# Optimization experiments

Hardware: AMD Instinct MI355X
Metric: run time of the kernel (lower is better)

The kernel has to match this reference:

```python
import jax, jax.numpy as jnp
import numpy as np

B, T, D, L, H = 8, 1024, 768, 8, 12
BLOCK_SIZE = 4
HD = D // H


def setup_inputs() -> dict:
    key = jax.random.key(0)
    ks = jax.random.split(key, 10)
    sd = 0.02
    return {
        "x_init": jax.random.normal(ks[0], (B, T, D), jnp.float32),
        "attn_proj_w": jax.random.normal(ks[1], (L, D), jnp.float32) * sd,
        "mlp_proj_w": jax.random.normal(ks[2], (L, D), jnp.float32) * sd,
        "Wqkv": jax.random.normal(ks[3], (L, D, 3 * D), jnp.float32) * sd,
        "Wo": jax.random.normal(ks[4], (L, D, D), jnp.float32) * sd,
        "Wm1": jax.random.normal(ks[5], (L, D, 4 * D), jnp.float32) * sd,
        "Wm2": jax.random.normal(ks[6], (L, 4 * D, D), jnp.float32) * sd,
        "attn_scale": 1.0 + jax.random.normal(ks[7], (L, D), jnp.float32) * sd,
        "mlp_scale": 1.0 + jax.random.normal(ks[8], (L, D), jnp.float32) * sd,
        "ln_s": jnp.ones((L,), jnp.float32),
    }


def _rms_norm(x):
    # F.rms_norm with eps=None -> eps = finfo(dtype).eps
    eps = jnp.finfo(x.dtype).eps
    return x * jax.lax.rsqrt(jnp.mean(x * x, axis=-1, keepdims=True) + eps)


def _aggregate(V, q):
    # V: [n, B, T, D]; scalar-query depth attention (keys RMS-normed, values raw)
    K = _rms_norm(V)
    logits = jnp.einsum('d,nbtd->nbt', q, K)
    w = jax.nn.softmax(logits, axis=0)
    return jnp.einsum('nbt,nbtd->btd', w, V)


def _mha(x, wqkv, wo):
    # causal multi-head self-attention
    b, t, d = x.shape
    qkv = x @ wqkv                                   # [b, t, 3D]
    q, k, v = jnp.split(qkv, 3, axis=-1)
    q = q.reshape(b, t, H, HD)
    k = k.reshape(b, t, H, HD)
    v = v.reshape(b, t, H, HD)
    scores = jnp.einsum('bqhd,bkhd->bhqk', q, k) / np.sqrt(HD).astype(np.float32)
    mask = jnp.tril(jnp.ones((t, t), bool))
    scores = jnp.where(mask[None, None], scores, jnp.asarray(-1e30, scores.dtype))
    attn = jax.nn.softmax(scores, axis=-1)
    out = jnp.einsum('bhqk,bkhd->bqhd', attn, v).reshape(b, t, d)
    return out @ wo


def reference(x_init, attn_proj_w, mlp_proj_w, Wqkv, Wo, Wm1, Wm2,
              attn_scale, mlp_scale, ln_s):
    boundary_every = max(1, BLOCK_SIZE // 2)
    hist = [x_init]          # committed block representations
    partial = x_init         # intra-block partial accumulator
    for l in range(L):
        s = ln_s[l]
        V = jnp.stack(hist + [partial], axis=0)          # [n_hist+1, B, T, D]
        h = _aggregate(V, attn_proj_w[l])
        if l % boundary_every == 0:
            hist.append(partial)
            partial = jnp.zeros_like(partial)
        attn_out = _mha(_rms_norm(h) * s, Wqkv[l], Wo[l])
        partial = partial + attn_scale[l][None, None, :] * attn_out
        V2 = jnp.stack(hist + [partial], axis=0)
        h = _aggregate(V2, mlp_proj_w[l])
        mlp_out = jax.nn.gelu((_rms_norm(h) * s) @ Wm1[l]) @ Wm2[l]
        partial = partial + mlp_scale[l][None, None, :] * mlp_out
    return partial
```

## Files before the change

### kernel.cpp

```cpp
#include <hip/hip_runtime.h>
#include <hip/hip_bf16.h>
#include <math.h>
#include <stdint.h>

#define D_MODEL 768
#define T_SEQ   1024
#define B_BATCH 8
#define NHEAD   12
#define HDIM    64
#define NLAYER  8

typedef unsigned short u16;
typedef __attribute__((ext_vector_type(8))) short bf16x8;
typedef __attribute__((ext_vector_type(4))) float f32x4;
typedef __attribute__((ext_vector_type(4))) uint32_t u32x4;

static constexpr size_t BTD  = (size_t)B_BATCH * T_SEQ * D_MODEL;
static constexpr int    ROWS = B_BATCH * T_SEQ;
static constexpr float  EPSF = 1.1920928955078125e-07f;


__device__ __forceinline__ u16 f2bf(float x) {
    __hip_bfloat16 h = __float2bfloat16(x);
    return __builtin_bit_cast(u16, h);
}
__device__ __forceinline__ float bf2f(u16 u) {
    __hip_bfloat16 h = __builtin_bit_cast(__hip_bfloat16, u);
    return __bfloat162float(h);
}
__device__ __forceinline__ void split_bf(float x, u16& hi, u16& lo) {
    hi = f2bf(x);
    lo = f2bf(x - bf2f(hi));
}
__device__ __forceinline__ uint32_t cvt_pk_bf16(float a, float b) {
    uint32_t r;
    asm("v_cvt_pk_bf16_f32 %0, %1, %2" : "=v"(r) : "v"(a), "v"(b));
    return r;
}
__device__ __forceinline__ f32x4 mfma16(bf16x8 a, bf16x8 b, f32x4 c) {
    return __builtin_amdgcn_mfma_f32_16x16x32_bf16(a, b, c, 0, 0, 0);
}

__device__ __forceinline__ void gl_lds16(const void* g, void* l) {
    auto gp = reinterpret_cast<const __attribute__((address_space(1))) char*>(
        reinterpret_cast<uintptr_t>(g));
    auto lp = reinterpret_cast<__attribute__((address_space(3))) char*>(
        static_cast<uint32_t>(reinterpret_cast<uintptr_t>(l)));
    __builtin_amdgcn_global_load_lds(gp, lp, 16, 0, 0);
}

__device__ __forceinline__ float block_reduce_sum(float v, float* sbuf) {
    #pragma unroll
    for (int off = 32; off > 0; off >>= 1) v += __shfl_down(v, off);
    __syncthreads();
    if ((threadIdx.x & 63) == 0) sbuf[threadIdx.x >> 6] = v;
    __syncthreads();
    return sbuf[0] + sbuf[1] + sbuf[2] + sbuf[3];
}

__device__ __forceinline__ float gelu_fast(float x) {
    float z = 0.7978845608028654f * (x + 0.044715f * x * x * x);
    float e = __expf(2.f * z);
    return x - x / (e + 1.f);
}

template<int N>
__global__ __launch_bounds__(256)
void agg_norm_kernel(const float* __restrict__ v0, const float* __restrict__ v1,
                     const float* __restrict__ v2, const float* __restrict__ v3,
                     const float* __restrict__ v4, const float* __restrict__ v5,
                     const float* __restrict__ q,  const float* __restrict__ lns,
                     u16* __restrict__ xh) {
    __shared__ float sbuf[4];
    const float* V[6] = {v0, v1, v2, v3, v4, v5};
    const size_t row = blockIdx.x;
    const int tid = threadIdx.x;

    float qv[3];
    #pragma unroll
    for (int j = 0; j < 3; ++j) qv[j] = q[tid + j * 256];

    float vv[N][3];
    float logits[N];
    #pragma unroll
    for (int i = 0; i < N; ++i) {
        const float* vr = V[i] + row * D_MODEL;
        float ssq = 0.f, qd = 0.f;
        #pragma unroll
        for (int j = 0; j < 3; ++j) {
            float x = vr[tid + j * 256];
            vv[i][j] = x;
            ssq = fmaf(x, x, ssq);
            qd  = fmaf(qv[j], x, qd);
        }
        float S  = block_reduce_sum(ssq, sbuf);
        float Qd = block_reduce_sum(qd,  sbuf);
        logits[i] = Qd * rsqrtf(S * (1.f / 768.f) + EPSF);
    }
    float mx = logits[0];
    #pragma unroll
    for (int i = 1; i < N; ++i) mx = fmaxf(mx, logits[i]);
    float w[N];
    float wsum = 0.f;
    #pragma unroll
    for (int i = 0; i < N; ++i) { w[i] = __expf(logits[i] - mx); wsum += w[i]; }
    float inv = 1.f / wsum;

    float outv[3] = {0.f, 0.f, 0.f};
    #pragma unroll
    for (int i = 0; i < N; ++i) {
        float wi = w[i] * inv;
        #pragma unroll
        for (int j = 0; j < 3; ++j) outv[j] = fmaf(wi, vv[i][j], outv[j]);
    }
    float ssq = 0.f;
    #pragma unroll
    for (int j = 0; j < 3; ++j) ssq = fmaf(outv[j], outv[j], ssq);
    float S2 = block_reduce_sum(ssq, sbuf);
    float scale = lns[0] * rsqrtf(S2 * (1.f / 768.f) + EPSF);
    #pragma unroll
    for (int j = 0; j < 3; ++j)
        xh[row * D_MODEL + tid + j * 256] = f2bf(outv[j] * scale);
}

__global__ __launch_bounds__(256)
void transpose_all(const float* __restrict__ Wqkv, const float* __restrict__ Wo,
                   const float* __restrict__ Wm1,  const float* __restrict__ Wm2,
                   u16* __restrict__ T0, u16* __restrict__ T1,
                   u16* __restrict__ T2, u16* __restrict__ T3) {
    const int id = blockIdx.x;
    const float* W; u16* Th; int K, N, t;
    if (id < 1728)      { W = Wqkv; Th = T0; K = 768;  N = 2304; t = id; }
    else if (id < 2304) { W = Wo;   Th = T1; K = 768;  N = 768;  t = id - 1728; }
    else if (id < 4608) { W = Wm1;  Th = T2; K = 768;  N = 3072; t = id - 2304; }
    else                { W = Wm2;  Th = T3; K = 3072; N = 768;  t = id - 4608; }
    const int nk = K >> 5;
    const int bk = (t % nk) * 32, bn = (t / nk) * 32;

    __shared__ float tt[32][33];
    const int r = threadIdx.x >> 3, c4 = (threadIdx.x & 7) * 4;
    float4 v = *(const float4*)&W[(size_t)(bk + r) * N + bn + c4];
    tt[r][c4 + 0] = v.x; tt[r][c4 + 1] = v.y; tt[r][c4 + 2] = v.z; tt[r][c4 + 3] = v.w;
    __syncthreads();
    u16 h[4];
    #pragma unroll
    for (int j = 0; j < 4; ++j) h[j] = f2bf(tt[c4 + j][r]);
    size_t o = (size_t)(bn + r) * K + bk + c4;
    *(uint2*)&Th[o] = make_uint2((uint32_t)h[0] | ((uint32_t)h[1] << 16),
                                 (uint32_t)h[2] | ((uint32_t)h[3] << 16));
}

__global__ __launch_bounds__(256)
void vt_transpose(const u16* __restrict__ vh, u16* __restrict__ vth) {
    __shared__ u16 th[32][36];
    const int bh = blockIdx.z;
    const int t0 = blockIdx.x * 32, d0 = blockIdx.y * 32;
    const int r = threadIdx.x >> 3, c = (threadIdx.x & 7) * 4;
    const size_t ib = ((size_t)(bh << 10) + t0 + r) * 64 + d0 + c;
    *(uint2*)&th[r][c] = *(const uint2*)&vh[ib];
    __syncthreads();
    const size_t ob = ((size_t)(bh << 6) + d0 + r) * 1024 + t0 + c;
    u16 a0 = th[c + 0][r], a1 = th[c + 1][r], a2 = th[c + 2][r], a3 = th[c + 3][r];
    *(uint2*)&vth[ob] = make_uint2((uint32_t)a0 | ((uint32_t)a1 << 16),
                                   (uint32_t)a2 | ((uint32_t)a3 << 16));
}

template<int EPI, int BN>
__global__ __launch_bounds__(256)
void gemm_bf1(const u16* __restrict__ Ah, const u16* __restrict__ Bh,
              float* __restrict__ Cf, u16* __restrict__ Ch,
              const float* __restrict__ scale, int M, int N, int K,
              u16* __restrict__ Qh, u16* __restrict__ Ql,
              u16* __restrict__ Kh, u16* __restrict__ Vh) {
    constexpr int NJ = BN / 32;
    constexpr int BUF_U16 = 4096 + BN * 32;
    __shared__ u16 smem[2 * BUF_U16];

    const int nwg = gridDim.x * gridDim.y;
    const int lin = blockIdx.y * gridDim.x + blockIdx.x;
    const int wg  = (lin & 7) * (nwg >> 3) + (lin >> 3);
    const int bm  = (wg / gridDim.x) << 7;
    const int bn  = (wg % gridDim.x) * BN;

    const int tid = threadIdx.x;
    const int w = tid >> 6, l = tid & 63;
    const int wr = w >> 1, wc = w & 1;

    const int grow = tid >> 2;
    const int gcol = (((tid & 3) ^ ((tid >> 3) & 3)) << 3);
    const size_t aoff0 = (size_t)(bm + grow) * K + gcol;
    const size_t boff0 = (size_t)(bn + grow) * K + gcol;
    const size_t s64 = (size_t)64 * K;
    char* sb0 = (char*)smem;
    char* sb1 = (char*)smem + 2 * BUF_U16;
    const uint32_t wq = (uint32_t)w << 10;

    auto stage = [&](char* sbuf, int k0) {
        gl_lds16(Ah + aoff0 + k0,       sbuf + 0    + wq);
        gl_lds16(Ah + aoff0 + s64 + k0, sbuf + 4096 + wq);
        gl_lds16(Bh + boff0 + k0,       sbuf + 8192 + wq);
        if constexpr (BN == 128)
            gl_lds16(Bh + boff0 + s64 + k0, sbuf + 12288 + wq);
    };

    f32x4 acc[4][NJ] = {};

    const int key8 = (((l & 15) >> 1) & 3) << 3;
    const int kswz = ((l >> 4) << 3) ^ key8;
    const int arow = wr * 64 + (l & 15);
    const int brow = wc * (BN / 2) + (l & 15);
    const int nk = K >> 5;

    stage(sb0, 0);
    for (int kt = 0; kt < nk; ++kt) {
        char* cur = (kt & 1) ? sb1 : sb0;
        char* nxt = (kt & 1) ? sb0 : sb1;
        if (kt + 1 < nk) {
            stage(nxt, (kt + 1) << 5);
            if constexpr (BN == 128)
                asm volatile("s_waitcnt vmcnt(4)\n\ts_barrier" ::: "memory");
            else
                asm volatile("s_waitcnt vmcnt(3)\n\ts_barrier" ::: "memory");
        } else {
            asm volatile("s_waitcnt vmcnt(0)\n\ts_barrier" ::: "memory");
        }
        __builtin_amdgcn_sched_barrier(0);

        const u16* bu = (const u16*)cur;
        bf16x8 ah[4], bh4[NJ];
        #pragma unroll
        for (int i = 0; i < 4; ++i)
            ah[i] = *(const bf16x8*)&bu[(arow + i * 16) * 32 + kswz];
        #pragma unroll
        for (int j = 0; j < NJ; ++j)
            bh4[j] = *(const bf16x8*)&bu[4096 + (brow + j * 16) * 32 + kswz];
        asm volatile("s_waitcnt lgkmcnt(0)" ::: "memory");
        __builtin_amdgcn_sched_barrier(0);
        asm volatile("s_barrier" ::: "memory");

        #pragma unroll
        for (int i = 0; i < 4; ++i) {
            #pragma unroll
            for (int j = 0; j < NJ; ++j)
                acc[i][j] = mfma16(ah[i], bh4[j], acc[i][j]);
        }
    }

    const int crow0 = bm + wr * 64 + ((l >> 4) << 2);
    const int ccol0 = bn + wc * (BN / 2) + (l & 15);
    #pragma unroll
    for (int i = 0; i < 4; ++i) {
        #pragma unroll
        for (int j = 0; j < NJ; ++j) {
            const int col = ccol0 + j * 16;
            #pragma unroll
            for (int r = 0; r < 4; ++r) {
                const int row = crow0 + i * 16 + r;
                const size_t o = (size_t)row * N + col;
                float v = acc[i][j][r];
                if (EPI == 1) {
                    Ch[o] = f2bf(gelu_fast(v));
                } else if (EPI == 2) {
                    Cf[o] += scale[col] * v;
                } else if (EPI == 4) {
                    Cf[o] = scale[col] * v;
                } else if (EPI == 3) {
                    const int which = (col >= 1536) ? 2 : ((col >= 768) ? 1 : 0);
                    const int hcol = col - which * 768;
                    const size_t dst = ((size_t)((row >> 10) * NHEAD + (hcol >> 6)) * 1024
                                        + (row & 1023)) * 64 + (hcol & 63);
                    if (which == 0) {
                        v *= 0.125f;
                        u16 hi, lo;
                        split_bf(v, hi, lo);
                        Qh[dst] = hi; Ql[dst] = lo;
                    } else if (which == 1) {
                        Kh[dst] = f2bf(v);
                    } else {
                        Vh[dst] = f2bf(v);
                    }
                }
            }
        }
    }
}

__global__ __launch_bounds__(256, 3)
void flash16(const u16* __restrict__ qh, const u16* __restrict__ ql,
             const u16* __restrict__ kh, const u16* __restrict__ vth,
             u16* __restrict__ ch) {
    const int id = blockIdx.x;
    const int r8 = id & 7, s = id >> 3;
    const int bh = r8 + 8 * (s >> 3);
    const int p  = s & 7;
    const int hh = bh % NHEAD, bb = bh / NHEAD;
    const int tid = threadIdx.x, w = tid >> 6, l = tid & 63;
    const int lq = l & 15, lg = l >> 4;
    const size_t hb = (size_t)bh << 16;

    const int wqA = p * 64 + w * 16;
    const int wqB = (15 - p) * 64 + w * 16;
    const int qA = wqA + lq, qB = wqB + lq;

    bf16x8 qA0, qA1, qA2, qA3, qB0, qB1, qB2, qB3;
    {
        const size_t qa = hb + ((size_t)qA << 6) + lg * 8;
        qA0 = *(const bf16x8*)(qh + qa);       qA1 = *(const bf16x8*)(ql + qa);
        qA2 = *(const bf16x8*)(qh + qa + 32);  qA3 = *(const bf16x8*)(ql + qa + 32);
        const size_t qb = hb + ((size_t)qB << 6) + lg * 8;
        qB0 = *(const bf16x8*)(qh + qb);       qB1 = *(const bf16x8*)(ql + qb);
        qB2 = *(const bf16x8*)(qh + qb + 32);  qB3 = *(const bf16x8*)(ql + qb + 32);
    }

    f32x4 oA[4] = {}, oB[4] = {};
    float mA = -30000.f, lsA = 0.f, mB = -30000.f, lsB = 0.f;
    const int ntiles = 32 - 2 * p;
    const int src0 = 32 * (lg & 1) + lq, src1 = src0 + 16;
    const bool hiHalf = lg >= 2;

    bf16x8 KA[4], KB[4], VA[4], VB[4];
    auto loadK = [&](bf16x8 (&K)[4], int k0) {
        const size_t kb0 = hb + (size_t)(k0 + lq) * 64 + lg * 8;
        const size_t kb1 = kb0 + 16 * 64;
        K[0] = *(const bf16x8*)(kh + kb0);
        K[1] = *(const bf16x8*)(kh + kb0 + 32);
        K[2] = *(const bf16x8*)(kh + kb1);
        K[3] = *(const bf16x8*)(kh + kb1 + 32);
    };
    auto loadV = [&](bf16x8 (&V)[4], int k0) {
        #pragma unroll
        for (int dt = 0; dt < 4; ++dt) {
            const size_t vb = hb + (size_t)(dt * 16 + lq) * 1024 + k0 + lg * 8;
            V[dt] = *(const bf16x8*)(vth + vb);
        }
    };

    auto path = [&](bf16x8 (&Kc)[4], bf16x8 (&vf)[4], int k0, int wqX, int qX,
                    bf16x8 q0, bf16x8 q1, bf16x8 q2, bf16x8 q3,
                    float& mX, float& lsX, f32x4 (&oX)[4]) {
        f32x4 s0 = {}, s1 = {};
        s0 = mfma16(Kc[0], q0, s0); s0 = mfma16(Kc[0], q1, s0);
        s0 = mfma16(Kc[1], q2, s0); s0 = mfma16(Kc[1], q3, s0);
        s1 = mfma16(Kc[2], q0, s1); s1 = mfma16(Kc[2], q1, s1);
        s1 = mfma16(Kc[3], q2, s1); s1 = mfma16(Kc[3], q3, s1);
        if (k0 + 31 > wqX) {
            #pragma unroll
            for (int r = 0; r < 4; ++r) {
                if (k0 + 4 * lg + r > qX)      s0[r] = -30000.f;
                if (k0 + 16 + 4 * lg + r > qX) s1[r] = -30000.f;
            }
        }
        float tmloc = fmaxf(fmaxf(fmaxf(s0[0], s0[1]), fmaxf(s0[2], s0[3])),
                            fmaxf(fmaxf(s1[0], s1[1]), fmaxf(s1[2], s1[3])));
        if (__any(tmloc > mX + 8.f)) {
            float tm = fmaxf(tmloc, __shfl_xor(tmloc, 16));
            tm = fmaxf(tm, __shfl_xor(tm, 32));
            const float mnew = fmaxf(mX, tm);
            const float fac = __expf(mX - mnew);
            mX = mnew;
            lsX *= fac;
            #pragma unroll
            for (int dt = 0; dt < 4; ++dt) {
                oX[dt][0] *= fac; oX[dt][1] *= fac;
                oX[dt][2] *= fac; oX[dt][3] *= fac;
            }
        }
        float ps = 0.f;
        #pragma unroll
        for (int r = 0; r < 4; ++r) {
            s0[r] = __expf(s0[r] - mX); ps += s0[r];
            s1[r] = __expf(s1[r] - mX); ps += s1[r];
        }
        lsX += ps;
        const uint32_t wA0 = cvt_pk_bf16(s0[0], s0[1]);
        const uint32_t wA1 = cvt_pk_bf16(s0[2], s0[3]);
        const uint32_t wB0 = cvt_pk_bf16(s1[0], s1[1]);
        const uint32_t wB1 = cvt_pk_bf16(s1[2], s1[3]);
        const uint32_t a0 = (uint32_t)__shfl((int)wA0, src0);
        const uint32_t b0 = (uint32_t)__shfl((int)wB0, src0);
        const uint32_t a1 = (uint32_t)__shfl((int)wA1, src0);
        const uint32_t b1 = (uint32_t)__shfl((int)wB1, src0);
        const uint32_t a2 = (uint32_t)__shfl((int)wA0, src1);
        const uint32_t b2 = (uint32_t)__shfl((int)wB0, src1);
        const uint32_t a3 = (uint32_t)__shfl((int)wA1, src1);
        const uint32_t b3 = (uint32_t)__shfl((int)wB1, src1);
        u32x4 pw = { hiHalf ? b0 : a0, hiHalf ? b1 : a1,
                     hiHalf ? b2 : a2, hiHalf ? b3 : a3 };
        const bf16x8 pb = __builtin_bit_cast(bf16x8, pw);
        #pragma unroll
        for (int dt = 0; dt < 4; ++dt)
            oX[dt] = mfma16(vf[dt], pb, oX[dt]);
    };

    auto step = [&](bf16x8 (&Kc)[4], bf16x8 (&Vc)[4],
                    bf16x8 (&Kn)[4], bf16x8 (&Vn)[4], int kt) {
        const int k0 = kt * 32;
        const int ktn = (kt + 1 < ntiles) ? kt + 1 : kt;
        loadK(Kn, ktn * 32);
        loadV(Vn, ktn * 32);
        if (k0 <= wqB + 15)
            path(Kc, Vc, k0, wqB, qB, qB0, qB1, qB2, qB3, mB, lsB, oB);
        if (k0 <= wqA + 15)
            path(Kc, Vc, k0, wqA, qA, qA0, qA1, qA2, qA3, mA, lsA, oA);
    };

    loadK(KA, 0);
    loadV(VA, 0);
    for (int kt = 0; kt < ntiles; kt += 2) {
        step(KA, VA, KB, VB, kt);
        step(KB, VB, KA, VA, kt + 1);
    }

    lsA += __shfl_xor(lsA, 16); lsA += __shfl_xor(lsA, 32);
    lsB += __shfl_xor(lsB, 16); lsB += __shfl_xor(lsB, 32);
    const float invA = 1.f / lsA, invB = 1.f / lsB;
    const size_t cbA = ((size_t)(bb * 1024 + qA)) * 768 + hh * 64;
    const size_t cbB = ((size_t)(bb * 1024 + qB)) * 768 + hh * 64;
    #pragma unroll
    for (int dt = 0; dt < 4; ++dt) {
        u16 h4[4];
        #pragma unroll
        for (int r = 0; r < 4; ++r) h4[r] = f2bf(oA[dt][r] * invA);
        size_t co = cbA + dt * 16 + 4 * lg;
        *(uint2*)&ch[co] = make_uint2((uint32_t)h4[0] | ((uint32_t)h4[1] << 16),
                                      (uint32_t)h4[2] | ((uint32_t)h4[3] << 16));
        #pragma unroll
        for (int r = 0; r < 4; ++r) h4[r] = f2bf(oB[dt][r] * invB);
        co = cbB + dt * 16 + 4 * lg;
        *(uint2*)&ch[co] = make_uint2((uint32_t)h4[0] | ((uint32_t)h4[1] << 16),
                                      (uint32_t)h4[2] | ((uint32_t)h4[3] << 16));
    }
}


extern "C" void kernel_launch(void* const* d_in, const int* in_sizes, int n_in,
                              void* d_out, int out_size, void* d_ws, size_t ws_size,
                              hipStream_t stream) {
    const float* x0     = (const float*)d_in[0];
    const float* aproj  = (const float*)d_in[1];
    const float* mproj  = (const float*)d_in[2];
    const float* Wqkv   = (const float*)d_in[3];
    const float* Wo     = (const float*)d_in[4];
    const float* Wm1    = (const float*)d_in[5];
    const float* Wm2    = (const float*)d_in[6];
    const float* ascale = (const float*)d_in[7];
    const float* mscale = (const float*)d_in[8];
    const float* lns    = (const float*)d_in[9];
    float* out = (float*)d_out;
    char*  base = (char*)d_ws;

    float* p1  = (float*)base;
    float* p2  = p1 + BTD;
    float* p3  = p2 + BTD;
    u16*   xnh = (u16*)(base + 12 * BTD);
    u16*   wt0 = (u16*)(base + 14 * BTD);
    u16*   wt1 = wt0 + (size_t)2304 * 768;
    u16*   wt2 = wt1 + (size_t)768 * 768;
    u16*   wt3 = wt2 + (size_t)3072 * 768;
    char*  QB  = (char*)(wt3 + (size_t)768 * 3072);
    u16* qh   = (u16*)QB;
    u16* ql   = qh  + BTD;
    u16* kh   = ql  + BTD;
    u16* vh   = kh  + BTD;
    u16* vth  = vh  + BTD;
    u16* ctxh = vh;
    u16* midh = qh;

    float* pb[3] = {p1, p2, p3};
    const float* hist[6];
    int nh = 1;
    hist[0] = x0;
    const float* partial_c = x0;
    float* partial_w = nullptr;
    int pidx = 0;

    auto launch_agg = [&](int n, const float* Vl6[6], const float* qvec,
                          const float* lnsl) {
        switch (n) {
        case 2: agg_norm_kernel<2><<<dim3(ROWS), 256, 0, stream>>>(Vl6[0], Vl6[1], Vl6[2], Vl6[3], Vl6[4], Vl6[5], qvec, lnsl, xnh); break;
        case 3: agg_norm_kernel<3><<<dim3(ROWS), 256, 0, stream>>>(Vl6[0], Vl6[1], Vl6[2], Vl6[3], Vl6[4], Vl6[5], qvec, lnsl, xnh); break;
        case 4: agg_norm_kernel<4><<<dim3(ROWS), 256, 0, stream>>>(Vl6[0], Vl6[1], Vl6[2], Vl6[3], Vl6[4], Vl6[5], qvec, lnsl, xnh); break;
        case 5: agg_norm_kernel<5><<<dim3(ROWS), 256, 0, stream>>>(Vl6[0], Vl6[1], Vl6[2], Vl6[3], Vl6[4], Vl6[5], qvec, lnsl, xnh); break;
        default: agg_norm_kernel<6><<<dim3(ROWS), 256, 0, stream>>>(Vl6[0], Vl6[1], Vl6[2], Vl6[3], Vl6[4], Vl6[5], qvec, lnsl, xnh); break;
        }
    };

    for (int l = 0; l < NLAYER; ++l) {
        transpose_all<<<dim3(6912), 256, 0, stream>>>(
            Wqkv + (size_t)l * D_MODEL * 3 * D_MODEL,
            Wo   + (size_t)l * D_MODEL * D_MODEL,
            Wm1  + (size_t)l * D_MODEL * 4 * D_MODEL,
            Wm2  + (size_t)l * 4 * D_MODEL * D_MODEL,
            wt0, wt1, wt2, wt3);

        const float* Vl6[6] = {nullptr, nullptr, nullptr, nullptr, nullptr, nullptr};
        for (int i = 0; i < nh; ++i) Vl6[i] = hist[i];
        Vl6[nh] = partial_c;
        launch_agg(nh + 1, Vl6, aproj + (size_t)l * D_MODEL, lns + l);

        const bool boundary = ((l & 1) == 0);
        if (boundary) {
            hist[nh++] = partial_c;
            float* np = (pidx < 3) ? pb[pidx] : out;
            ++pidx;
            partial_w = np;
            partial_c = np;
        }

        gemm_bf1<3, 128><<<dim3(3 * D_MODEL / 128, ROWS / 128), 256, 0, stream>>>(
            xnh, wt0, nullptr, nullptr, nullptr,
            ROWS, 3 * D_MODEL, D_MODEL, qh, ql, kh, vh);

        vt_transpose<<<dim3(T_SEQ / 32, HDIM / 32, B_BATCH * NHEAD), 256, 0, stream>>>(
            vh, vth);

        flash16<<<dim3(768), 256, 0, stream>>>(qh, ql, kh, vth, ctxh);

        if (boundary)
            gemm_bf1<4, 64><<<dim3(D_MODEL / 64, ROWS / 128), 256, 0, stream>>>(
                ctxh, wt1, partial_w, nullptr,
                ascale + (size_t)l * D_MODEL, ROWS, D_MODEL, D_MODEL,
                nullptr, nullptr, nullptr, nullptr);
        else
            gemm_bf1<2, 64><<<dim3(D_MODEL / 64, ROWS / 128), 256, 0, stream>>>(
                ctxh, wt1, partial_w, nullptr,
                ascale + (size_t)l * D_MODEL, ROWS, D_MODEL, D_MODEL,
                nullptr, nullptr, nullptr, nullptr);

        const float* V26[6] = {nullptr, nullptr, nullptr, nullptr, nullptr, nullptr};
        for (int i = 0; i < nh; ++i) V26[i] = hist[i];
        V26[nh] = partial_c;
        launch_agg(nh + 1, V26, mproj + (size_t)l * D_MODEL, lns + l);

        gemm_bf1<1, 128><<<dim3(4 * D_MODEL / 128, ROWS / 128), 256, 0, stream>>>(
            xnh, wt2, nullptr, midh,
            nullptr, ROWS, 4 * D_MODEL, D_MODEL,
            nullptr, nullptr, nullptr, nullptr);
        gemm_bf1<2, 64><<<dim3(D_MODEL / 64, ROWS / 128), 256, 0, stream>>>(
            midh, wt3, partial_w, nullptr,
            mscale + (size_t)l * D_MODEL, ROWS, D_MODEL, 4 * D_MODEL,
            nullptr, nullptr, nullptr, nullptr);
    }
}
```

Measured before the change: 2.862 ms.

## Deduplicate repeated aggregation inputs and split-K the second MLP GEMM

Because x_init is always present twice in the history, the aggregation kernel now reads it once and doubles its softmax weight. This removes one full-activation read per aggregation launch, and layer 0 takes a trivial single-input path. The down-projection GEMM (K=3072) is split into two K halves that accumulate into the residual with float atomics, doubling the block count. The atomics add read-modify-write traffic and make the summation order nondeterministic.

```diff
diff --git a/kernel.cpp b/kernel.cpp
--- a/kernel.cpp
+++ b/kernel.cpp
@@ -68,50 +68,58 @@
 __global__ __launch_bounds__(256)
 void agg_norm_kernel(const float* __restrict__ v0, const float* __restrict__ v1,
                      const float* __restrict__ v2, const float* __restrict__ v3,
-                     const float* __restrict__ v4, const float* __restrict__ v5,
+                     const float* __restrict__ v4,
                      const float* __restrict__ q,  const float* __restrict__ lns,
                      u16* __restrict__ xh) {
     __shared__ float sbuf[4];
-    const float* V[6] = {v0, v1, v2, v3, v4, v5};
+    const float* V[5] = {v0, v1, v2, v3, v4};
     const size_t row = blockIdx.x;
     const int tid = threadIdx.x;
 
-    float qv[3];
-    #pragma unroll
-    for (int j = 0; j < 3; ++j) qv[j] = q[tid + j * 256];
-
-    float vv[N][3];
-    float logits[N];
-    #pragma unroll
-    for (int i = 0; i < N; ++i) {
-        const float* vr = V[i] + row * D_MODEL;
-        float ssq = 0.f, qd = 0.f;
-        #pragma unroll
-        for (int j = 0; j < 3; ++j) {
-            float x = vr[tid + j * 256];
-            vv[i][j] = x;
-            ssq = fmaf(x, x, ssq);
-            qd  = fmaf(qv[j], x, qd);
-        }
-        float S  = block_reduce_sum(ssq, sbuf);
-        float Qd = block_reduce_sum(qd,  sbuf);
-        logits[i] = Qd * rsqrtf(S * (1.f / 768.f) + EPSF);
-    }
-    float mx = logits[0];
-    #pragma unroll
-    for (int i = 1; i < N; ++i) mx = fmaxf(mx, logits[i]);
-    float w[N];
-    float wsum = 0.f;
-    #pragma unroll
-    for (int i = 0; i < N; ++i) { w[i] = __expf(logits[i] - mx); wsum += w[i]; }
-    float inv = 1.f / wsum;
-
-    float outv[3] = {0.f, 0.f, 0.f};
-    #pragma unroll
-    for (int i = 0; i < N; ++i) {
-        float wi = w[i] * inv;
-        #pragma unroll
-        for (int j = 0; j < 3; ++j) outv[j] = fmaf(wi, vv[i][j], outv[j]);
+    float outv[3];
+    if constexpr (N == 1) {
+        #pragma unroll
+        for (int j = 0; j < 3; ++j) outv[j] = v0[row * D_MODEL + tid + j * 256];
+    } else {
+        float qv[3];
+        #pragma unroll
+        for (int j = 0; j < 3; ++j) qv[j] = q[tid + j * 256];
+
+        float vv[N][3];
+        float logits[N];
+        #pragma unroll
+        for (int i = 0; i < N; ++i) {
+            const float* vr = V[i] + row * D_MODEL;
+            float ssq = 0.f, qd = 0.f;
+            #pragma unroll
+            for (int j = 0; j < 3; ++j) {
+                float x = vr[tid + j * 256];
+                vv[i][j] = x;
+                ssq = fmaf(x, x, ssq);
+                qd  = fmaf(qv[j], x, qd);
+            }
+            float S  = block_reduce_sum(ssq, sbuf);
+            float Qd = block_reduce_sum(qd,  sbuf);
+            logits[i] = Qd * rsqrtf(S * (1.f / 768.f) + EPSF);
+        }
+        float mx = logits[0];
+        #pragma unroll
+        for (int i = 1; i < N; ++i) mx = fmaxf(mx, logits[i]);
+        float w[N];
+        #pragma unroll
+        for (int i = 0; i < N; ++i) w[i] = __expf(logits[i] - mx);
+        w[0] *= 2.f;
+        float wsum = 0.f;
+        #pragma unroll
+        for (int i = 0; i < N; ++i) wsum += w[i];
+        float inv = 1.f / wsum;
+        outv[0] = outv[1] = outv[2] = 0.f;
+        #pragma unroll
+        for (int i = 0; i < N; ++i) {
+            float wi = w[i] * inv;
+            #pragma unroll
+            for (int j = 0; j < 3; ++j) outv[j] = fmaf(wi, vv[i][j], outv[j]);
+        }
     }
     float ssq = 0.f;
     #pragma unroll
@@ -165,7 +173,7 @@
                                    (uint32_t)a2 | ((uint32_t)a3 << 16));
 }
 
-template<int EPI, int BN>
+template<int EPI, int BN, int KS>
 __global__ __launch_bounds__(256)
 void gemm_bf1(const u16* __restrict__ Ah, const u16* __restrict__ Bh,
               float* __restrict__ Cf, u16* __restrict__ Ch,
@@ -176,11 +184,13 @@
     constexpr int BUF_U16 = 4096 + BN * 32;
     __shared__ u16 smem[2 * BUF_U16];
 
-    const int nwg = gridDim.x * gridDim.y;
-    const int lin = blockIdx.y * gridDim.x + blockIdx.x;
+    const int gx = gridDim.x, gy = gridDim.y;
+    const int nwg = gx * gy * KS;
+    const int lin = (blockIdx.z * gy + blockIdx.y) * gx + blockIdx.x;
     const int wg  = (lin & 7) * (nwg >> 3) + (lin >> 3);
-    const int bm  = (wg / gridDim.x) << 7;
-    const int bn  = (wg % gridDim.x) * BN;
+    const int bn  = (wg % gx) * BN;
+    const int bm  = ((wg / gx) % gy) << 7;
+    const int kz  = wg / (gx * gy);
 
     const int tid = threadIdx.x;
     const int w = tid >> 6, l = tid & 63;
@@ -209,14 +219,15 @@
     const int kswz = ((l >> 4) << 3) ^ key8;
     const int arow = wr * 64 + (l & 15);
     const int brow = wc * (BN / 2) + (l & 15);
-    const int nk = K >> 5;
-
-    stage(sb0, 0);
-    for (int kt = 0; kt < nk; ++kt) {
+    const int nk2 = (K >> 5) / KS;
+    const int kt0 = kz * nk2;
+
+    stage(sb0, kt0 << 5);
+    for (int kt = 0; kt < nk2; ++kt) {
         char* cur = (kt & 1) ? sb1 : sb0;
         char* nxt = (kt & 1) ? sb0 : sb1;
-        if (kt + 1 < nk) {
-            stage(nxt, (kt + 1) << 5);
+        if (kt + 1 < nk2) {
+            stage(nxt, (kt0 + kt + 1) << 5);
             if constexpr (BN == 128)
                 asm volatile("s_waitcnt vmcnt(4)\n\ts_barrier" ::: "memory");
             else
@@ -264,6 +275,8 @@
                     Cf[o] += scale[col] * v;
                 } else if (EPI == 4) {
                     Cf[o] = scale[col] * v;
+                } else if (EPI == 5) {
+                    unsafeAtomicAdd(&Cf[o], scale[col] * v);
                 } else if (EPI == 3) {
                     const int which = (col >= 1536) ? 2 : ((col >= 768) ? 1 : 0);
                     const int hcol = col - which * 768;
@@ -467,21 +480,23 @@
     u16* midh = qh;
 
     float* pb[3] = {p1, p2, p3};
-    const float* hist[6];
-    int nh = 1;
-    hist[0] = x0;
-    const float* partial_c = x0;
+    const float* L[5] = {x0, nullptr, nullptr, nullptr, nullptr};
+    int nL = 1;
     float* partial_w = nullptr;
     int pidx = 0;
 
-    auto launch_agg = [&](int n, const float* Vl6[6], const float* qvec,
-                          const float* lnsl) {
-        switch (n) {
-        case 2: agg_norm_kernel<2><<<dim3(ROWS), 256, 0, stream>>>(Vl6[0], Vl6[1], Vl6[2], Vl6[3], Vl6[4], Vl6[5], qvec, lnsl, xnh); break;
-        case 3: agg_norm_kernel<3><<<dim3(ROWS), 256, 0, stream>>>(Vl6[0], Vl6[1], Vl6[2], Vl6[3], Vl6[4], Vl6[5], qvec, lnsl, xnh); break;
-        case 4: agg_norm_kernel<4><<<dim3(ROWS), 256, 0, stream>>>(Vl6[0], Vl6[1], Vl6[2], Vl6[3], Vl6[4], Vl6[5], qvec, lnsl, xnh); break;
-        case 5: agg_norm_kernel<5><<<dim3(ROWS), 256, 0, stream>>>(Vl6[0], Vl6[1], Vl6[2], Vl6[3], Vl6[4], Vl6[5], qvec, lnsl, xnh); break;
-        default: agg_norm_kernel<6><<<dim3(ROWS), 256, 0, stream>>>(Vl6[0], Vl6[1], Vl6[2], Vl6[3], Vl6[4], Vl6[5], qvec, lnsl, xnh); break;
+    auto launch_agg = [&](const float* qvec, const float* lnsl) {
+        const float* a = L[0];
+        const float* b = (nL > 1) ? L[1] : nullptr;
+        const float* c = (nL > 2) ? L[2] : nullptr;
+        const float* d = (nL > 3) ? L[3] : nullptr;
+        const float* e = (nL > 4) ? L[4] : nullptr;
+        switch (nL) {
+        case 1: agg_norm_kernel<1><<<dim3(ROWS), 256, 0, stream>>>(a, b, c, d, e, qvec, lnsl, xnh); break;
+        case 2: agg_norm_kernel<2><<<dim3(ROWS), 256, 0, stream>>>(a, b, c, d, e, qvec, lnsl, xnh); break;
+        case 3: agg_norm_kernel<3><<<dim3(ROWS), 256, 0, stream>>>(a, b, c, d, e, qvec, lnsl, xnh); break;
+        case 4: agg_norm_kernel<4><<<dim3(ROWS), 256, 0, stream>>>(a, b, c, d, e, qvec, lnsl, xnh); break;
+        default: agg_norm_kernel<5><<<dim3(ROWS), 256, 0, stream>>>(a, b, c, d, e, qvec, lnsl, xnh); break;
         }
     };
 
@@ -493,21 +508,17 @@
             Wm2  + (size_t)l * 4 * D_MODEL * D_MODEL,
             wt0, wt1, wt2, wt3);
 
-        const float* Vl6[6] = {nullptr, nullptr, nullptr, nullptr, nullptr, nullptr};
-        for (int i = 0; i < nh; ++i) Vl6[i] = hist[i];
-        Vl6[nh] = partial_c;
-        launch_agg(nh + 1, Vl6, aproj + (size_t)l * D_MODEL, lns + l);
+        launch_agg(aproj + (size_t)l * D_MODEL, lns + l);
 
         const bool boundary = ((l & 1) == 0);
         if (boundary) {
-            hist[nh++] = partial_c;
             float* np = (pidx < 3) ? pb[pidx] : out;
             ++pidx;
             partial_w = np;
-            partial_c = np;
-        }
-
-        gemm_bf1<3, 128><<<dim3(3 * D_MODEL / 128, ROWS / 128), 256, 0, stream>>>(
+            L[nL++] = np;
+        }
+
+        gemm_bf1<3, 128, 1><<<dim3(3 * D_MODEL / 128, ROWS / 128), 256, 0, stream>>>(
             xnh, wt0, nullptr, nullptr, nullptr,
             ROWS, 3 * D_MODEL, D_MODEL, qh, ql, kh, vh);
 
@@ -517,26 +528,23 @@
         flash16<<<dim3(768), 256, 0, stream>>>(qh, ql, kh, vth, ctxh);
 
         if (boundary)
-            gemm_bf1<4, 64><<<dim3(D_MODEL / 64, ROWS / 128), 256, 0, stream>>>(
+            gemm_bf1<4, 64, 1><<<dim3(D_MODEL / 64, ROWS / 128), 256, 0, stream>>>(
                 ctxh, wt1, partial_w, nullptr,
                 ascale + (size_t)l * D_MODEL, ROWS, D_MODEL, D_MODEL,
                 nullptr, nullptr, nullptr, nullptr);
         else
-            gemm_bf1<2, 64><<<dim3(D_MODEL / 64, ROWS / 128), 256, 0, stream>>>(
+            gemm_bf1<2, 64, 1><<<dim3(D_MODEL / 64, ROWS / 128), 256, 0, stream>>>(
                 ctxh, wt1, partial_w, nullptr,
                 ascale + (size_t)l * D_MODEL, ROWS, D_MODEL, D_MODEL,
                 nullptr, nullptr, nullptr, nullptr);
 
-        const float* V26[6] = {nullptr, nullptr, nullptr, nullptr, nullptr, nullptr};
-        for (int i = 0; i < nh; ++i) V26[i] = hist[i];
-        V26[nh] = partial_c;
-        launch_agg(nh + 1, V26, mproj + (size_t)l * D_MODEL, lns + l);
-
-        gemm_bf1<1, 128><<<dim3(4 * D_MODEL / 128, ROWS / 128), 256, 0, stream>>>(
+        launch_agg(mproj + (size_t)l * D_MODEL, lns + l);
+
+        gemm_bf1<1, 128, 1><<<dim3(4 * D_MODEL / 128, ROWS / 128), 256, 0, stream>>>(
             xnh, wt2, nullptr, midh,
             nullptr, ROWS, 4 * D_MODEL, D_MODEL,
             nullptr, nullptr, nullptr, nullptr);
-        gemm_bf1<2, 64><<<dim3(D_MODEL / 64, ROWS / 128), 256, 0, stream>>>(
+        gemm_bf1<5, 64, 2><<<dim3(D_MODEL / 64, ROWS / 128, 2), 256, 0, stream>>>(
             midh, wt3, partial_w, nullptr,
             mscale + (size_t)l * D_MODEL, ROWS, D_MODEL, 4 * D_MODEL,
             nullptr, nullptr, nullptr, nullptr);
```

Measured after the change: 2.889 ms. No clear change (+0.9%).
